# Kernel tuning notes

Hardware: AMD Instinct MI355X
Metric: run time of the kernel (lower is better)

## Reference

```python
import jax, jax.numpy as jnp
import numpy as np

B, N, C = 8, 729, 1152
H, D = 16, 72          # num_heads, head_dim (C = H*D)
F = 4304               # intermediate_size
R = 23                 # ToMe merge count r
EPS = 1e-6
SCALE = D ** -0.5


def _ln(x, g, b):
    m = jnp.mean(x, axis=-1, keepdims=True)
    v = jnp.var(x, axis=-1, keepdims=True)
    return (x - m) * jax.lax.rsqrt(v + EPS) * g + b


def _tome_merge_wavg(metric, x, r):
    """ToMe bipartite soft matching + weighted-average merge (size=None -> ones).
    metric: [B,N,D] per-token key mean; x: [B,N,C]. Returns [B, N-r, C]."""
    m = metric / jnp.linalg.norm(metric, axis=-1, keepdims=True)
    a, bm = m[:, ::2], m[:, 1::2]                       # [B,Na,D],[B,Nb,D]
    scores = jnp.einsum('bnd,bmd->bnm', a, bm)          # cosine sims [B,Na,Nb]
    node_max = jnp.max(scores, axis=-1)                 # [B,Na]
    node_idx = jnp.argmax(scores, axis=-1)              # best dst per src
    edge_idx = jnp.argsort(-node_max, axis=-1)          # descending similarity
    unm_idx = edge_idx[:, r:]                           # unmerged src tokens
    src_idx = edge_idx[:, :r]                           # merged src tokens
    dst_idx = jnp.take_along_axis(node_idx, src_idx, axis=1)  # [B,r]

    size = jnp.ones(x.shape[:2] + (1,), x.dtype)

    def merge_sum(t):
        src, dst = t[:, ::2], t[:, 1::2]
        unm = jnp.take_along_axis(src, unm_idx[..., None], axis=1)
        sel = jnp.take_along_axis(src, src_idx[..., None], axis=1)
        dst = jax.vmap(lambda d, i, s: d.at[i].add(s))(dst, dst_idx, sel)
        return jnp.concatenate([unm, dst], axis=1)

    xs = merge_sum(x * size)
    ss = merge_sum(size)
    return xs / ss


def setup_inputs() -> dict:
    key = jax.random.key(0)
    ks = jax.random.split(key, 16)
    s = 0.02
    inp = {
        'hidden_states': jax.random.normal(ks[0], (B, N, C), jnp.float32),
        'attention_mask': 0.1 * jax.random.normal(ks[1], (B, 1, N, N), jnp.float32),
        'wq': s * jax.random.normal(ks[2], (C, C), jnp.float32),
        'bq': jnp.zeros((C,), jnp.float32),
        'wk': s * jax.random.normal(ks[3], (C, C), jnp.float32),
        'bk': jnp.zeros((C,), jnp.float32),
        'wv': s * jax.random.normal(ks[4], (C, C), jnp.float32),
        'bv': jnp.zeros((C,), jnp.float32),
        'wo': s * jax.random.normal(ks[5], (C, C), jnp.float32),
        'bo': jnp.zeros((C,), jnp.float32),
        'ln1_w': jnp.ones((C,), jnp.float32),
        'ln1_b': jnp.zeros((C,), jnp.float32),
        'ln2_w': jnp.ones((C,), jnp.float32),
        'ln2_b': jnp.zeros((C,), jnp.float32),
        'fc1_w': s * jax.random.normal(ks[6], (C, F), jnp.float32),
        'fc1_b': jnp.zeros((F,), jnp.float32),
        'fc2_w': s * jax.random.normal(ks[7], (F, C), jnp.float32),
        'fc2_b': jnp.zeros((C,), jnp.float32),
    }
    return inp


def reference(hidden_states, attention_mask, wq, bq, wk, bk, wv, bv, wo, bo,
              ln1_w, ln1_b, ln2_w, ln2_b, fc1_w, fc1_b, fc2_w, fc2_b):
    residual = hidden_states
    x = _ln(hidden_states, ln1_w, ln1_b)

    q = (x @ wq + bq).reshape(B, N, H, D)
    k = (x @ wk + bk).reshape(B, N, H, D)
    v = (x @ wv + bv).reshape(B, N, H, D)

    metric = jnp.mean(k, axis=2)                        # [B,N,D] (mean over heads)

    scores = jnp.einsum('bqhd,bkhd->bhqk', q, k) * SCALE
    scores = scores + attention_mask                    # [B,1,N,N] broadcast bias
    attn = jax.nn.softmax(scores.astype(jnp.float32), axis=-1).astype(q.dtype)
    out = jnp.einsum('bhqk,bkhd->bqhd', attn, v).reshape(B, N, C)
    attn_out = out @ wo + bo

    h = residual + attn_out
    h = _tome_merge_wavg(metric, h, R)                  # [B, N-R, C]

    residual = h
    h = _ln(h, ln2_w, ln2_b)
    h = jax.nn.gelu(h @ fc1_w + fc1_b, approximate=True)  # gelu_pytorch_tanh
    h = h @ fc2_w + fc2_b
    return residual + h
```

## Files before the change

kernel.cpp:

```cpp
#include <hip/hip_runtime.h>
#include <hip/hip_bf16.h>
#include <math.h>

namespace {

constexpr int Bn = 8;
constexpr int Nn = 729;
constexpr int Cn = 1152;
constexpr int Hn = 16;
constexpr int Dn = 72;
constexpr int Fn = 4304;
constexpr int Rn = 23;
constexpr int NAn = 365;
constexpr int NBn = 364;
constexpr int NMn = 706;
constexpr int UNMn = NAn - Rn;
constexpr float EPSf = 1e-6f;
constexpr float SCALEf = 0.11785113019775793f;

using bf16 = __hip_bfloat16;
typedef short v8s __attribute__((ext_vector_type(8)));
typedef float v4f __attribute__((ext_vector_type(4)));

__device__ __forceinline__ float toF(bf16 v) { return __bfloat162float(v); }
__device__ __forceinline__ void stF(float* p, float v) { *p = v; }
__device__ __forceinline__ void stF(bf16* p, float v) { *p = __float2bfloat16(v); }

__device__ __forceinline__ float geluf(float x) {
  float x3 = x * x * x;
  return 0.5f * x * (1.f + tanhf(0.7978845608028654f * (x + 0.044715f * x3)));
}

__device__ __forceinline__ int clampi(int v, int lo, int hi) {
  return v < lo ? lo : (v > hi ? hi : v);
}

__global__ __launch_bounds__(256) void ln_stats_kernel(const float* __restrict__ x,
                                                       float* __restrict__ sf,
                                                       double* __restrict__ sd,
                                                       int rows) {
  int row = blockIdx.x;
  if (row >= rows) return;
  const float* xr = x + (size_t)row * Cn;
  double s = 0.0, s2 = 0.0;
  for (int c = threadIdx.x; c < Cn; c += 256) {
    double v = (double)xr[c];
    s += v; s2 += v * v;
  }
  __shared__ double sh[8];
#pragma unroll
  for (int o = 32; o > 0; o >>= 1) { s += __shfl_down(s, o); s2 += __shfl_down(s2, o); }
  int w = threadIdx.x >> 6;
  if ((threadIdx.x & 63) == 0) { sh[w] = s; sh[4 + w] = s2; }
  __syncthreads();
  if (threadIdx.x == 0) {
    double ts = sh[0] + sh[1] + sh[2] + sh[3];
    double ts2 = sh[4] + sh[5] + sh[6] + sh[7];
    double mean = ts / Cn;
    double var = ts2 / Cn - mean * mean;
    double rstd = 1.0 / sqrt(var + (double)EPSf);
    sf[2 * row] = (float)mean;
    sf[2 * row + 1] = (float)rstd;
    if (sd) { sd[2 * row] = mean; sd[2 * row + 1] = rstd; }
  }
}

__global__ __launch_bounds__(256) void ln_apply_kernel(const float* __restrict__ x,
                                                       const float* __restrict__ stats,
                                                       const float* __restrict__ g,
                                                       const float* __restrict__ b,
                                                       bf16* __restrict__ y) {
  int row = blockIdx.x;
  float mean = stats[2 * row], rstd = stats[2 * row + 1];
  const float* xr = x + (size_t)row * Cn;
  bf16* yr = y + (size_t)row * Cn;
  for (int c = threadIdx.x; c < Cn; c += 256)
    yr[c] = __float2bfloat16((xr[c] - mean) * rstd * g[c] + b[c]);
}

__global__ __launch_bounds__(256) void wconv_kernel(const float* __restrict__ W,
                                                    bf16* __restrict__ Wt,
                                                    int K, int N, float scale) {
  __shared__ float tile[32][33];
  int kt = blockIdx.y * 32, nt = blockIdx.x * 32;
  int tx = threadIdx.x & 31, ty = threadIdx.x >> 5;
#pragma unroll
  for (int yy = 0; yy < 4; ++yy) {
    int k = kt + ty * 4 + yy, n = nt + tx;
    tile[ty * 4 + yy][tx] = (k < K && n < N) ? W[(size_t)k * N + n] : 0.f;
  }
  __syncthreads();
#pragma unroll
  for (int yy = 0; yy < 4; ++yy) {
    int n = nt + ty * 4 + yy, k = kt + tx;
    if (n < N && k < K) Wt[(size_t)n * K + k] = __float2bfloat16(tile[tx][ty * 4 + yy] * scale);
  }
}

__global__ __launch_bounds__(256) void vscale_kernel(const float* __restrict__ in,
                                                     float* __restrict__ out, int n, float s) {
  int i = blockIdx.x * 256 + threadIdx.x;
  if (i < n) out[i] = in[i] * s;
}

template <typename OT, int BT>
__global__ __launch_bounds__(256) void mfma_gemm(const bf16* __restrict__ A,
                                                 const bf16* __restrict__ Wt,
                                                 const float* __restrict__ bias,
                                                 const float* __restrict__ resid,
                                                 OT* __restrict__ Cout,
                                                 int M, int N, int K, int act) {
  constexpr int FR = BT / 32;
  constexpr int PASSES = BT / 64;
  __align__(16) __shared__ short As[BT * 40];
  __align__(16) __shared__ short Bs[BT * 40];
  int bm = blockIdx.y * BT, bn = blockIdx.x * BT;
  int tid = threadIdx.x;
  int lane = tid & 63, w = tid >> 6;
  int wm = w >> 1, wn = w & 1;
  int l16 = lane & 15, quad = lane >> 4;
  int srow = tid >> 2, skc = (tid & 3) * 8;
  v4f acc[FR][FR];
#pragma unroll
  for (int i = 0; i < FR; ++i)
#pragma unroll
    for (int j = 0; j < FR; ++j) acc[i][j] = (v4f){0.f, 0.f, 0.f, 0.f};
  int ksteps = (K + 31) / 32;
  for (int ks = 0; ks < ksteps; ++ks) {
    int k0 = ks * 32;
    __syncthreads();
#pragma unroll
    for (int h = 0; h < PASSES; ++h) {
      int r = srow + h * 64;
      int4 za = {0, 0, 0, 0}, zb = {0, 0, 0, 0};
      if (k0 + skc < K) {
        if (bm + r < M) za = *reinterpret_cast<const int4*>(A + (size_t)(bm + r) * K + k0 + skc);
        if (bn + r < N) zb = *reinterpret_cast<const int4*>(Wt + (size_t)(bn + r) * K + k0 + skc);
      }
      *reinterpret_cast<int4*>(&As[r * 40 + skc]) = za;
      *reinterpret_cast<int4*>(&Bs[r * 40 + skc]) = zb;
    }
    __syncthreads();
    v8s af[FR], bfr[FR];
#pragma unroll
    for (int i = 0; i < FR; ++i)
      af[i] = *reinterpret_cast<const v8s*>(&As[(wm * (BT / 2) + i * 16 + l16) * 40 + quad * 8]);
#pragma unroll
    for (int j = 0; j < FR; ++j)
      bfr[j] = *reinterpret_cast<const v8s*>(&Bs[(wn * (BT / 2) + j * 16 + l16) * 40 + quad * 8]);
#pragma unroll
    for (int i = 0; i < FR; ++i)
#pragma unroll
      for (int j = 0; j < FR; ++j)
        acc[i][j] = __builtin_amdgcn_mfma_f32_16x16x32_bf16(af[i], bfr[j], acc[i][j], 0, 0, 0);
  }
#pragma unroll
  for (int i = 0; i < FR; ++i) {
#pragma unroll
    for (int j = 0; j < FR; ++j) {
#pragma unroll
      for (int r = 0; r < 4; ++r) {
        int row = bm + wm * (BT / 2) + i * 16 + quad * 4 + r;
        int col = bn + wn * (BT / 2) + j * 16 + l16;
        if (row < M && col < N) {
          float v = acc[i][j][r] + bias[col];
          if (act) v = geluf(v);
          if (resid) v += resid[(size_t)row * N + col];
          stF(&Cout[(size_t)row * N + col], v);
        }
      }
    }
  }
}

constexpr int NKP = 768;
__global__ __launch_bounds__(256) void vtrans_kernel(const bf16* __restrict__ v,
                                                     bf16* __restrict__ vt) {
  int kb = blockIdx.x % 12;
  int bh = blockIdx.x / 12;
  int h = bh % Hn, b = bh / Hn;
  __shared__ short Ts[64][73];
  int tid = threadIdx.x;
#pragma unroll
  for (int i = 0; i < 18; ++i) {
    int idx = tid + i * 256;
    int key = idx / 72, d = idx % 72;
    int kg = kb * 64 + key;
    bf16 val = (kg < Nn) ? v[((size_t)(b * Nn + kg)) * Cn + h * Dn + d] : bf16(0.f);
    Ts[key][d] = *reinterpret_cast<short*>(&val);
  }
  __syncthreads();
#pragma unroll
  for (int i = 0; i < 18; ++i) {
    int idx = tid + i * 256;
    int d = idx / 64, key = idx % 64;
    vt[((size_t)bh * 80 + d) * NKP + kb * 64 + key] = *reinterpret_cast<bf16*>(&Ts[key][d]);
  }
  for (int i = tid; i < 8 * 64; i += 256) {
    int d = 72 + i / 64, key = i % 64;
    vt[((size_t)bh * 80 + d) * NKP + kb * 64 + key] = bf16(0.f);
  }
}

constexpr int ATQ = 64, ATK = 64;
constexpr int NQT2 = (Nn + ATQ - 1) / ATQ;
constexpr int NKT = 12;
constexpr int KSS = 104, VTS = 72, PSS = 72;

__device__ __forceinline__ void attn_load_tile(const bf16* __restrict__ k,
                                               const bf16* __restrict__ vt,
                                               int b, int bh, int h, int kt_, int tid,
                                               int4* kr, int4* vr) {
#pragma unroll
  for (int i = 0; i < 3; ++i) {
    int idx = tid + i * 256;
    int r = idx / 12, ch = idx % 12;
    int kg = kt_ + r;
    int4 z = {0, 0, 0, 0};
    if (ch < 9 && kg < Nn)
      z = *reinterpret_cast<const int4*>(k + ((size_t)(b * Nn + kg)) * Cn + h * Dn + ch * 8);
    kr[i] = z;
    if (idx < 640) {
      int d = idx >> 3, kc = idx & 7;
      vr[i] = *reinterpret_cast<const int4*>(vt + ((size_t)bh * 80 + d) * NKP + kt_ + kc * 8);
    }
  }
}

__global__ __launch_bounds__(256) void attn_mfma_kernel(bf16* q ,
                                                        const bf16* __restrict__ k,
                                                        const bf16* __restrict__ vt,
                                                        const float* __restrict__ mask) {
  int blk = blockIdx.x;
  int qt = blk % NQT2;
  int bh = blk / NQT2;
  int h = bh % Hn;
  int b = bh / Hn;
  __align__(16) __shared__ short Ks[ATK * KSS];
  __align__(16) __shared__ short Vt[80 * VTS];
  __align__(16) __shared__ short Ps[4][16 * PSS];
  int tid = threadIdx.x;
  int lane = tid & 63, w = tid >> 6;
  int l16 = lane & 15, quad = lane >> 4;

  v8s aq[3];
  int qg_l = qt * ATQ + w * 16 + l16;
  {
    const bf16* qrow = q + ((size_t)(b * Nn + (qg_l < Nn ? qg_l : 0))) * Cn + h * Dn;
#pragma unroll
    for (int ks = 0; ks < 3; ++ks) {
      bool valid = (qg_l < Nn) && (ks < 2 || quad == 0);
      if (valid)
        aq[ks] = *reinterpret_cast<const v8s*>(qrow + ks * 32 + quad * 8);
      else
        aq[ks] = (v8s){0, 0, 0, 0, 0, 0, 0, 0};
    }
  }

  v4f o[5];
#pragma unroll
  for (int dj = 0; dj < 5; ++dj) o[dj] = (v4f){0.f, 0.f, 0.f, 0.f};
  float m_r[4] = {-INFINITY, -INFINITY, -INFINITY, -INFINITY};
  float l_r[4] = {0.f, 0.f, 0.f, 0.f};

  int4 kr[3], vr[3];
  attn_load_tile(k, vt, b, bh, h, 0, tid, kr, vr);

  for (int t = 0; t < NKT; ++t) {
    int kt2 = t * ATK;
    __syncthreads();
#pragma unroll
    for (int i = 0; i < 3; ++i) {
      int idx = tid + i * 256;
      int r = idx / 12, ch = idx % 12;
      *reinterpret_cast<int4*>(&Ks[r * KSS + ch * 8]) = kr[i];
      if (idx < 640) {
        int d = idx >> 3, kc = idx & 7;
        *reinterpret_cast<int4*>(&Vt[d * VTS + kc * 8]) = vr[i];
      }
    }
    __syncthreads();
    if (t + 1 < NKT) attn_load_tile(k, vt, b, bh, h, kt2 + ATK, tid, kr, vr);

    v4f sfr[4];
#pragma unroll
    for (int j = 0; j < 4; ++j) sfr[j] = (v4f){0.f, 0.f, 0.f, 0.f};
#pragma unroll
    for (int ks = 0; ks < 3; ++ks) {
#pragma unroll
      for (int j = 0; j < 4; ++j) {
        v8s bk_ = *reinterpret_cast<const v8s*>(&Ks[(j * 16 + l16) * KSS + ks * 32 + quad * 8]);
        sfr[j] = __builtin_amdgcn_mfma_f32_16x16x32_bf16(aq[ks], bk_, sfr[j], 0, 0, 0);
      }
    }
    float sv[4][4];
    int qbase = qt * ATQ + w * 16 + quad * 4;
    bool tfull = (kt2 + ATK <= Nn);
#pragma unroll
    for (int r = 0; r < 4; ++r) {
      int qg = qbase + r;
      const float* mrow = mask + ((size_t)(b * Nn + (qg < Nn ? qg : 0))) * Nn;
      if (tfull && qg < Nn) {
#pragma unroll
        for (int j = 0; j < 4; ++j) sv[j][r] = sfr[j][r] + mrow[kt2 + j * 16 + l16];
      } else {
#pragma unroll
        for (int j = 0; j < 4; ++j) {
          int kg = kt2 + j * 16 + l16;
          sv[j][r] = (kg < Nn && qg < Nn) ? sfr[j][r] + mrow[kg] : -INFINITY;
        }
      }
    }
    float alpha[4];
#pragma unroll
    for (int r = 0; r < 4; ++r) {
      float mx = fmaxf(fmaxf(sv[0][r], sv[1][r]), fmaxf(sv[2][r], sv[3][r]));
#pragma unroll
      for (int o2 = 1; o2 < 16; o2 <<= 1) mx = fmaxf(mx, __shfl_xor(mx, o2));
      float mnew = fmaxf(m_r[r], mx);
      float ps = 0.f;
#pragma unroll
      for (int j = 0; j < 4; ++j) {
        float p = __expf(sv[j][r] - mnew);
        bf16 pb = __float2bfloat16(p);
        Ps[w][(quad * 4 + r) * PSS + j * 16 + l16] = *reinterpret_cast<short*>(&pb);
        ps += p;
      }
#pragma unroll
      for (int o2 = 1; o2 < 16; o2 <<= 1) ps += __shfl_xor(ps, o2);
      alpha[r] = __expf(m_r[r] - mnew);
      l_r[r] = l_r[r] * alpha[r] + ps;
      m_r[r] = mnew;
    }
#pragma unroll
    for (int dj = 0; dj < 5; ++dj)
#pragma unroll
      for (int r = 0; r < 4; ++r) o[dj][r] *= alpha[r];
#pragma unroll
    for (int st = 0; st < 2; ++st) {
      v8s ap = *reinterpret_cast<const v8s*>(&Ps[w][l16 * PSS + st * 32 + quad * 8]);
#pragma unroll
      for (int dj = 0; dj < 5; ++dj) {
        v8s bv_ = *reinterpret_cast<const v8s*>(&Vt[(dj * 16 + l16) * VTS + st * 32 + quad * 8]);
        o[dj] = __builtin_amdgcn_mfma_f32_16x16x32_bf16(ap, bv_, o[dj], 0, 0, 0);
      }
    }
  }
  float linv[4];
#pragma unroll
  for (int r = 0; r < 4; ++r) linv[r] = (l_r[r] > 0.f) ? 1.f / l_r[r] : 0.f;
#pragma unroll
  for (int dj = 0; dj < 5; ++dj) {
    int d = dj * 16 + l16;
    if (d >= Dn) continue;
#pragma unroll
    for (int r = 0; r < 4; ++r) {
      int qg = qt * ATQ + w * 16 + quad * 4 + r;
      if (qg < Nn)
        q[((size_t)(b * Nn + qg)) * Cn + h * Dn + d] = __float2bfloat16(o[dj][r] * linv[r]);
    }
  }
}

__global__ __launch_bounds__(128) void wkavg_kernel(const float* __restrict__ wk,
                                                    const float* __restrict__ bk,
                                                    double* __restrict__ wka,
                                                    double* __restrict__ bka) {
  int c = blockIdx.x;
  int d = threadIdx.x;
  if (d < Dn) {
    double s = 0.0;
    for (int h = 0; h < Hn; ++h) s += (double)wk[(size_t)c * Cn + h * Dn + d];
    wka[(size_t)c * Dn + d] = s / Hn;
    if (c == 0) {
      double t = 0.0;
      for (int h = 0; h < Hn; ++h) t += (double)bk[h * Dn + d];
      bka[d] = t / Hn;
    }
  }
}

constexpr int MT_ROWS = 64;
constexpr int MT_KT = 32;
constexpr int MT_SK = 3;
constexpr int MT_KC = Cn / MT_SK;
__global__ __launch_bounds__(256) void metric_gemm_kernel(const float* __restrict__ x,
                                                          const double* __restrict__ sd,
                                                          const float* __restrict__ g,
                                                          const float* __restrict__ b,
                                                          const double* __restrict__ wka,
                                                          double* __restrict__ kpart,
                                                          int rows) {
  int row0 = blockIdx.x * MT_ROWS;
  int k0base = blockIdx.y * MT_KC;
  __shared__ double As[MT_ROWS][MT_KT + 1];
  __shared__ double Ws[MT_KT][Dn];
  __shared__ double smean[MT_ROWS], srstd[MT_ROWS];
  int tid = threadIdx.x;
  int rg = tid >> 3;
  int dg = tid & 7;
  int d0 = dg * 9;
  if (tid < MT_ROWS) {
    int r = row0 + tid;
    smean[tid] = (r < rows) ? sd[2 * r] : 0.0;
    srstd[tid] = (r < rows) ? sd[2 * r + 1] : 0.0;
  }
  double acc0[9], acc1[9];
#pragma unroll
  for (int j = 0; j < 9; ++j) { acc0[j] = 0.0; acc1[j] = 0.0; }
  __syncthreads();
  for (int kt = 0; kt < MT_KC; kt += MT_KT) {
    int k0 = k0base + kt;
    __syncthreads();
#pragma unroll
    for (int i = 0; i < 8; ++i) {
      int idx = tid + i * 256;
      int c = idx & 31, r = idx >> 5;
      int gr = row0 + r;
      double a = 0.0;
      if (gr < rows) {
        double xv = (double)x[(size_t)gr * Cn + k0 + c];
        a = (xv - smean[r]) * srstd[r] * (double)g[k0 + c] + (double)b[k0 + c];
      }
      As[r][c] = a;
    }
#pragma unroll
    for (int i = 0; i < 9; ++i) {
      int idx = tid + i * 256;
      int c = idx / Dn, d = idx % Dn;
      Ws[c][d] = wka[(size_t)(k0 + c) * Dn + d];
    }
    __syncthreads();
#pragma unroll 2
    for (int c = 0; c < MT_KT; ++c) {
      double a0 = As[rg * 2][c], a1 = As[rg * 2 + 1][c];
#pragma unroll
      for (int j = 0; j < 9; ++j) {
        double wv = Ws[c][d0 + j];
        acc0[j] += a0 * wv;
        acc1[j] += a1 * wv;
      }
    }
  }
  size_t base = (size_t)blockIdx.y * rows;
  int r0g = row0 + rg * 2;
#pragma unroll
  for (int j = 0; j < 9; ++j) {
    if (r0g < rows) kpart[(base + r0g) * Dn + d0 + j] = acc0[j];
    if (r0g + 1 < rows) kpart[(base + r0g + 1) * Dn + d0 + j] = acc1[j];
  }
}

__global__ __launch_bounds__(128) void metric_norm_kernel(const double* __restrict__ kpart,
                                                          const double* __restrict__ bka,
                                                          double* __restrict__ mn,
                                                          int rows) {
  int row = blockIdx.x;
  __shared__ double red[Dn];
  __shared__ double nrm;
  int d = threadIdx.x;
  double v = 0.0;
  if (d < Dn) {
    v = kpart[(size_t)row * Dn + d]
      + kpart[((size_t)rows + row) * Dn + d]
      + kpart[((size_t)2 * rows + row) * Dn + d]
      + bka[d];
    red[d] = v * v;
  }
  __syncthreads();
  if (threadIdx.x == 0) {
    double t = 0.0;
    for (int i = 0; i < Dn; ++i) t += red[i];
    nrm = 1.0 / sqrt(t > 0.0 ? t : 1e-300);
  }
  __syncthreads();
  if (d < Dn) mn[(size_t)row * Dn + d] = v * nrm;
}

__global__ __launch_bounds__(128) void tome_score_kernel(const double* __restrict__ mn,
                                                         double* __restrict__ nmax,
                                                         int* __restrict__ nidx) {
  int blk = blockIdx.x;
  int i = blk % NAn;
  int b = blk / NAn;
  __shared__ double av[Dn];
  __shared__ double sv[128];
  __shared__ int si[128];
  int tid = threadIdx.x;
  if (tid < Dn) av[tid] = mn[((size_t)(b * Nn) + 2 * i) * Dn + tid];
  __syncthreads();
  double best = -1e300;
  int bi = 0;
  for (int c2 = tid; c2 < NBn; c2 += 128) {
    const double* bv = mn + ((size_t)(b * Nn) + 2 * c2 + 1) * Dn;
    double s = 0.0;
#pragma unroll 8
    for (int dd = 0; dd < Dn; ++dd) s += av[dd] * bv[dd];
    if (s > best) { best = s; bi = c2; }
  }
  sv[tid] = best;
  si[tid] = bi;
  __syncthreads();
  if (tid == 0) {
    double bb = sv[0];
    int ii = si[0];
    for (int t2 = 1; t2 < 128; ++t2) {
      if (sv[t2] > bb || (sv[t2] == bb && si[t2] < ii)) { bb = sv[t2]; ii = si[t2]; }
    }
    nmax[b * NAn + i] = bb;
    nidx[b * NAn + i] = clampi(ii, 0, NBn - 1);
  }
}

__global__ __launch_bounds__(512) void tome_sort_kernel(const double* __restrict__ nmax,
                                                        const int* __restrict__ nidx,
                                                        int* __restrict__ unm,
                                                        int* __restrict__ srcI,
                                                        int* __restrict__ dstI,
                                                        float* __restrict__ cnt) {
  int b = blockIdx.x;
  __shared__ double v[NAn];
  __shared__ int eidx[NAn];
  __shared__ int dsts[Rn];
  int tid = threadIdx.x;
  for (int i = tid; i < NAn; i += blockDim.x) {
    v[i] = nmax[b * NAn + i];
    eidx[i] = i;
  }
  __syncthreads();
  for (int i = tid; i < NAn; i += blockDim.x) {
    double vi = v[i];
    int rank = 0;
    for (int j = 0; j < NAn; ++j) {
      double vj = v[j];
      rank += (vj > vi) || (vj == vi && j < i);
    }
    eidx[clampi(rank, 0, NAn - 1)] = i;
  }
  __syncthreads();
  for (int r2 = tid; r2 < NAn; r2 += blockDim.x) {
    if (r2 >= Rn) unm[(size_t)b * UNMn + (r2 - Rn)] = clampi(eidx[r2], 0, NAn - 1);
  }
  if (tid < Rn) {
    int s = clampi(eidx[tid], 0, NAn - 1);
    srcI[b * Rn + tid] = s;
    int dd = clampi(nidx[b * NAn + s], 0, NBn - 1);
    dsts[tid] = dd;
    dstI[b * Rn + tid] = dd;
  }
  for (int j = tid; j < NBn; j += blockDim.x) cnt[(size_t)b * NBn + j] = 1.f;
  __syncthreads();
  if (tid == 0) {
    for (int r2 = 0; r2 < Rn; ++r2) cnt[(size_t)b * NBn + dsts[r2]] += 1.f;
  }
}

__global__ __launch_bounds__(256) void tome_merge_kernel(const float* __restrict__ h,
                                                         const int* __restrict__ unm,
                                                         const int* __restrict__ srcI,
                                                         const int* __restrict__ dstI,
                                                         const float* __restrict__ cnt,
                                                         float* __restrict__ mg) {
  int blk = blockIdx.x;
  int t = blk % NMn;
  int b = blk / NMn;
  __shared__ int s_src[Rn], s_dst[Rn];
  if (threadIdx.x < Rn) {
    s_src[threadIdx.x] = clampi(srcI[b * Rn + threadIdx.x], 0, NAn - 1);
    s_dst[threadIdx.x] = clampi(dstI[b * Rn + threadIdx.x], 0, NBn - 1);
  }
  __syncthreads();
  if (t < UNMn) {
    int tok = clampi(2 * clampi(unm[(size_t)b * UNMn + t], 0, NAn - 1), 0, Nn - 1);
    for (int c = threadIdx.x; c < Cn; c += 256)
      mg[((size_t)(b * NMn + t)) * Cn + c] = h[((size_t)(b * Nn + tok)) * Cn + c];
  } else {
    int j = t - UNMn;
    int tok = 2 * j + 1;
    float inv = 1.f / cnt[b * NBn + j];
    for (int c = threadIdx.x; c < Cn; c += 256) {
      float vsum = h[((size_t)(b * Nn + tok)) * Cn + c];
      for (int r2 = 0; r2 < Rn; ++r2)
        if (s_dst[r2] == j) vsum += h[((size_t)(b * Nn + 2 * s_src[r2])) * Cn + c];
      mg[((size_t)(b * NMn + t)) * Cn + c] = vsum * inv;
    }
  }
}

inline int cdiv(int a, int b) { return (a + b - 1) / b; }

}

extern "C" void kernel_launch(void* const* d_in, const int* in_sizes, int n_in,
                              void* d_out, int out_size, void* d_ws, size_t ws_size,
                              hipStream_t stream) {
  const float* hidden = (const float*)d_in[0];
  const float* mask   = (const float*)d_in[1];
  const float* wq = (const float*)d_in[2];
  const float* bq = (const float*)d_in[3];
  const float* wk = (const float*)d_in[4];
  const float* bk = (const float*)d_in[5];
  const float* wv = (const float*)d_in[6];
  const float* bv = (const float*)d_in[7];
  const float* wo = (const float*)d_in[8];
  const float* bo = (const float*)d_in[9];
  const float* ln1w = (const float*)d_in[10];
  const float* ln1b = (const float*)d_in[11];
  const float* ln2w = (const float*)d_in[12];
  const float* ln2b = (const float*)d_in[13];
  const float* fc1w = (const float*)d_in[14];
  const float* fc1b = (const float*)d_in[15];
  const float* fc2w = (const float*)d_in[16];
  const float* fc2b = (const float*)d_in[17];
  float* out = (float*)d_out;
  (void)in_sizes; (void)n_in; (void)out_size; (void)ws_size;

  char* ws = (char*)d_ws;
  size_t off = 0;
  auto alloc = [&](size_t nbytes) -> void* {
    void* p = ws + off;
    off += (nbytes + 255) & ~(size_t)255;
    return p;
  };
  int rows = Bn * Nn;
  int mrows = Bn * NMn;
  size_t bnc = (size_t)rows * Cn;
  bf16* wqT = (bf16*)alloc((size_t)Cn * Cn * 2);
  bf16* wkT = (bf16*)alloc((size_t)Cn * Cn * 2);
  bf16* wvT = (bf16*)alloc((size_t)Cn * Cn * 2);
  bf16* woT = (bf16*)alloc((size_t)Cn * Cn * 2);
  bf16* fc1T = (bf16*)alloc((size_t)Fn * Cn * 2);
  bf16* fc2T = (bf16*)alloc((size_t)Cn * Fn * 2);
  bf16* xlnB = (bf16*)alloc(bnc * 2);
  bf16* qb = (bf16*)alloc(bnc * 2);
  bf16* kb = (bf16*)alloc(bnc * 2);
  bf16* vb = (bf16*)alloc(bnc * 2);
  bf16* h2B = (bf16*)alloc((size_t)mrows * Cn * 2);
  constexpr int CHUNK = 2824;
  bf16* ffnB = (bf16*)alloc((size_t)CHUNK * Fn * 2);
  double* mnD = (double*)alloc((size_t)rows * Dn * 8);
  double* wkavgD = (double*)alloc((size_t)Cn * Dn * 8);
  double* bkavgD = (double*)alloc((size_t)Dn * 8);
  float* stats1f = (float*)alloc((size_t)rows * 2 * 4);
  double* stats1d = (double*)alloc((size_t)rows * 2 * 8);
  float* stats2f = (float*)alloc((size_t)mrows * 2 * 4);
  double* nmaxD = (double*)alloc((size_t)Bn * NAn * 8);
  int* nidx = (int*)alloc((size_t)Bn * NAn * 4);
  int* unm  = (int*)alloc((size_t)Bn * UNMn * 4);
  int* srcI = (int*)alloc((size_t)Bn * Rn * 4);
  int* dstI = (int*)alloc((size_t)Bn * Rn * 4);
  float* cnt = (float*)alloc((size_t)Bn * NBn * 4);
  float* bqS = (float*)alloc((size_t)Cn * 4);
  float* hbuf = (float*)kb;
  float* mg   = (float*)xlnB;
  bf16* vtG   = ffnB;
  double* kpartD = (double*)ffnB;

  wconv_kernel<<<dim3(cdiv(Cn, 32), cdiv(Cn, 32)), 256, 0, stream>>>(wq, wqT, Cn, Cn, SCALEf);
  wconv_kernel<<<dim3(cdiv(Cn, 32), cdiv(Cn, 32)), 256, 0, stream>>>(wk, wkT, Cn, Cn, 1.f);
  wconv_kernel<<<dim3(cdiv(Cn, 32), cdiv(Cn, 32)), 256, 0, stream>>>(wv, wvT, Cn, Cn, 1.f);
  wconv_kernel<<<dim3(cdiv(Cn, 32), cdiv(Cn, 32)), 256, 0, stream>>>(wo, woT, Cn, Cn, 1.f);
  wconv_kernel<<<dim3(cdiv(Fn, 32), cdiv(Cn, 32)), 256, 0, stream>>>(fc1w, fc1T, Cn, Fn, 1.f);
  wconv_kernel<<<dim3(cdiv(Cn, 32), cdiv(Fn, 32)), 256, 0, stream>>>(fc2w, fc2T, Fn, Cn, 1.f);
  vscale_kernel<<<cdiv(Cn, 256), 256, 0, stream>>>(bq, bqS, Cn, SCALEf);

  ln_stats_kernel<<<rows, 256, 0, stream>>>(hidden, stats1f, stats1d, rows);

  wkavg_kernel<<<Cn, 128, 0, stream>>>(wk, bk, wkavgD, bkavgD);
  metric_gemm_kernel<<<dim3(cdiv(rows, MT_ROWS), MT_SK), 256, 0, stream>>>(
      hidden, stats1d, ln1w, ln1b, wkavgD, kpartD, rows);
  metric_norm_kernel<<<rows, 128, 0, stream>>>(kpartD, bkavgD, mnD, rows);
  tome_score_kernel<<<Bn * NAn, 128, 0, stream>>>(mnD, nmaxD, nidx);
  tome_sort_kernel<<<Bn, 512, 0, stream>>>(nmaxD, nidx, unm, srcI, dstI, cnt);

  ln_apply_kernel<<<rows, 256, 0, stream>>>(hidden, stats1f, ln1w, ln1b, xlnB);

  dim3 g64(cdiv(Cn, 64), cdiv(rows, 64));
  mfma_gemm<bf16, 64><<<g64, 256, 0, stream>>>(xlnB, wqT, bqS, nullptr, qb, rows, Cn, Cn, 0);
  mfma_gemm<bf16, 64><<<g64, 256, 0, stream>>>(xlnB, wkT, bk, nullptr, kb, rows, Cn, Cn, 0);
  mfma_gemm<bf16, 64><<<g64, 256, 0, stream>>>(xlnB, wvT, bv, nullptr, vb, rows, Cn, Cn, 0);

  vtrans_kernel<<<Bn * Hn * 12, 256, 0, stream>>>(vb, vtG);

  attn_mfma_kernel<<<Bn * Hn * NQT2, 256, 0, stream>>>(qb, kb, vtG, mask);

  mfma_gemm<float, 64><<<g64, 256, 0, stream>>>(qb, woT, bo, hidden, hbuf, rows, Cn, Cn, 0);

  tome_merge_kernel<<<Bn * NMn, 256, 0, stream>>>(hbuf, unm, srcI, dstI, cnt, mg);

  ln_stats_kernel<<<mrows, 256, 0, stream>>>(mg, stats2f, (double*)nullptr, mrows);
  ln_apply_kernel<<<mrows, 256, 0, stream>>>(mg, stats2f, ln2w, ln2b, h2B);

  for (int c0 = 0; c0 < mrows; c0 += CHUNK) {
    int m = (mrows - c0 < CHUNK) ? (mrows - c0) : CHUNK;
    dim3 gf1(cdiv(Fn, 128), cdiv(m, 128));
    mfma_gemm<bf16, 128><<<gf1, 256, 0, stream>>>(h2B + (size_t)c0 * Cn, fc1T, fc1b, nullptr,
                                                  ffnB, m, Fn, Cn, 1);
    dim3 gf2(cdiv(Cn, 64), cdiv(m, 64));
    mfma_gemm<float, 64><<<gf2, 256, 0, stream>>>(ffnB, fc2T, fc2b, mg + (size_t)c0 * Cn,
                                                  out + (size_t)c0 * Cn, m, Cn, Fn, 0);
  }
}
```

Measured before the change: 1.174 ms.

## Use direct global-to-LDS loads in GEMM, remap attention blocks, enlarge FFN chunk

The GEMM tile loader now issues global_load_lds 16-byte transfers straight into unpadded shared memory for interior tiles, skipping the register round trip. Edge tiles keep the old guarded path. Removing the 40-short row padding may add LDS bank conflicts on fragment reads. The attention kernel interleaves batch as the fastest block index, which should change L2 locality for the mask. The per-iteration row-sum shuffle reduction is deferred to the end, and the FFN chunk size grows to all rows when the workspace is large enough, cutting chunk launches.

```diff
diff --git a/kernel.cpp b/kernel.cpp
--- a/kernel.cpp
+++ b/kernel.cpp
@@ -35,6 +35,12 @@
   return v < lo ? lo : (v > hi ? hi : v);
 }
 
+__device__ __forceinline__ void gl_lds16(const bf16* __restrict__ g, short* l) {
+  __builtin_amdgcn_global_load_lds(
+      (const __attribute__((address_space(1))) void*)g,
+      (__attribute__((address_space(3))) void*)l, 16, 0, 0);
+}
+
 __global__ __launch_bounds__(256) void ln_stats_kernel(const float* __restrict__ x,
                                                        float* __restrict__ sf,
                                                        double* __restrict__ sd,
@@ -111,15 +117,17 @@
                                                  OT* __restrict__ Cout,
                                                  int M, int N, int K, int act) {
   constexpr int FR = BT / 32;
-  constexpr int PASSES = BT / 64;
-  __align__(16) __shared__ short As[BT * 40];
-  __align__(16) __shared__ short Bs[BT * 40];
+  constexpr int WL = BT / 64;
+  __align__(16) __shared__ short As[BT * 32];
+  __align__(16) __shared__ short Bs[BT * 32];
   int bm = blockIdx.y * BT, bn = blockIdx.x * BT;
   int tid = threadIdx.x;
   int lane = tid & 63, w = tid >> 6;
   int wm = w >> 1, wn = w & 1;
   int l16 = lane & 15, quad = lane >> 4;
   int srow = tid >> 2, skc = (tid & 3) * 8;
+  int lr = lane >> 2, lc8 = (lane & 3) * 8;
+  bool interior = (bm + BT <= M) && (bn + BT <= N);
   v4f acc[FR][FR];
 #pragma unroll
   for (int i = 0; i < FR; ++i)
@@ -129,25 +137,35 @@
   for (int ks = 0; ks < ksteps; ++ks) {
     int k0 = ks * 32;
     __syncthreads();
-#pragma unroll
-    for (int h = 0; h < PASSES; ++h) {
-      int r = srow + h * 64;
-      int4 za = {0, 0, 0, 0}, zb = {0, 0, 0, 0};
-      if (k0 + skc < K) {
-        if (bm + r < M) za = *reinterpret_cast<const int4*>(A + (size_t)(bm + r) * K + k0 + skc);
-        if (bn + r < N) zb = *reinterpret_cast<const int4*>(Wt + (size_t)(bn + r) * K + k0 + skc);
-      }
-      *reinterpret_cast<int4*>(&As[r * 40 + skc]) = za;
-      *reinterpret_cast<int4*>(&Bs[r * 40 + skc]) = zb;
+    if (interior && (k0 + 32 <= K)) {
+#pragma unroll
+      for (int h2 = 0; h2 < WL; ++h2) {
+        int rb = (w + h2 * 4) * 16;
+        int r = rb + lr;
+        gl_lds16(A + (size_t)(bm + r) * K + k0 + lc8, &As[rb * 32]);
+        gl_lds16(Wt + (size_t)(bn + r) * K + k0 + lc8, &Bs[rb * 32]);
+      }
+    } else {
+#pragma unroll
+      for (int h2 = 0; h2 < WL; ++h2) {
+        int r = srow + h2 * 64;
+        int4 za = {0, 0, 0, 0}, zb = {0, 0, 0, 0};
+        if (k0 + skc < K) {
+          if (bm + r < M) za = *reinterpret_cast<const int4*>(A + (size_t)(bm + r) * K + k0 + skc);
+          if (bn + r < N) zb = *reinterpret_cast<const int4*>(Wt + (size_t)(bn + r) * K + k0 + skc);
+        }
+        *reinterpret_cast<int4*>(&As[r * 32 + skc]) = za;
+        *reinterpret_cast<int4*>(&Bs[r * 32 + skc]) = zb;
+      }
     }
     __syncthreads();
     v8s af[FR], bfr[FR];
 #pragma unroll
     for (int i = 0; i < FR; ++i)
-      af[i] = *reinterpret_cast<const v8s*>(&As[(wm * (BT / 2) + i * 16 + l16) * 40 + quad * 8]);
+      af[i] = *reinterpret_cast<const v8s*>(&As[(wm * (BT / 2) + i * 16 + l16) * 32 + quad * 8]);
 #pragma unroll
     for (int j = 0; j < FR; ++j)
-      bfr[j] = *reinterpret_cast<const v8s*>(&Bs[(wn * (BT / 2) + j * 16 + l16) * 40 + quad * 8]);
+      bfr[j] = *reinterpret_cast<const v8s*>(&Bs[(wn * (BT / 2) + j * 16 + l16) * 32 + quad * 8]);
 #pragma unroll
     for (int i = 0; i < FR; ++i)
 #pragma unroll
@@ -232,10 +250,11 @@
                                                         const bf16* __restrict__ vt,
                                                         const float* __restrict__ mask) {
   int blk = blockIdx.x;
-  int qt = blk % NQT2;
-  int bh = blk / NQT2;
-  int h = bh % Hn;
-  int b = bh / Hn;
+  int b = blk & 7;
+  int r0 = blk >> 3;
+  int h = r0 / NQT2;
+  int qt = r0 % NQT2;
+  int bh = b * Hn + h;
   __align__(16) __shared__ short Ks[ATK * KSS];
   __align__(16) __shared__ short Vt[80 * VTS];
   __align__(16) __shared__ short Ps[4][16 * PSS];
@@ -326,8 +345,6 @@
         Ps[w][(quad * 4 + r) * PSS + j * 16 + l16] = *reinterpret_cast<short*>(&pb);
         ps += p;
       }
-#pragma unroll
-      for (int o2 = 1; o2 < 16; o2 <<= 1) ps += __shfl_xor(ps, o2);
       alpha[r] = __expf(m_r[r] - mnew);
       l_r[r] = l_r[r] * alpha[r] + ps;
       m_r[r] = mnew;
@@ -348,7 +365,12 @@
   }
   float linv[4];
 #pragma unroll
-  for (int r = 0; r < 4; ++r) linv[r] = (l_r[r] > 0.f) ? 1.f / l_r[r] : 0.f;
+  for (int r = 0; r < 4; ++r) {
+    float lt = l_r[r];
+#pragma unroll
+    for (int o2 = 1; o2 < 16; o2 <<= 1) lt += __shfl_xor(lt, o2);
+    linv[r] = (lt > 0.f) ? 1.f / lt : 0.f;
+  }
 #pragma unroll
   for (int dj = 0; dj < 5; ++dj) {
     int d = dj * 16 + l16;
@@ -613,7 +635,7 @@
   const float* fc2w = (const float*)d_in[16];
   const float* fc2b = (const float*)d_in[17];
   float* out = (float*)d_out;
-  (void)in_sizes; (void)n_in; (void)out_size; (void)ws_size;
+  (void)in_sizes; (void)n_in; (void)out_size;
 
   char* ws = (char*)d_ws;
   size_t off = 0;
@@ -636,8 +658,6 @@
   bf16* kb = (bf16*)alloc(bnc * 2);
   bf16* vb = (bf16*)alloc(bnc * 2);
   bf16* h2B = (bf16*)alloc((size_t)mrows * Cn * 2);
-  constexpr int CHUNK = 2824;
-  bf16* ffnB = (bf16*)alloc((size_t)CHUNK * Fn * 2);
   double* mnD = (double*)alloc((size_t)rows * Dn * 8);
   double* wkavgD = (double*)alloc((size_t)Cn * Dn * 8);
   double* bkavgD = (double*)alloc((size_t)Dn * 8);
@@ -651,6 +671,10 @@
   int* dstI = (int*)alloc((size_t)Bn * Rn * 4);
   float* cnt = (float*)alloc((size_t)Bn * NBn * 4);
   float* bqS = (float*)alloc((size_t)Cn * 4);
+  bf16* ffnB = (bf16*)(ws + off);
+  size_t remain = (ws_size > off) ? (ws_size - off) : 0;
+  size_t fullB = (size_t)mrows * Fn * 2;
+  int CHUNK = (remain >= fullB) ? mrows : 2824;
   float* hbuf = (float*)kb;
   float* mg   = (float*)xlnB;
   bf16* vtG   = ffnB;
```

New measurement: 1.133 ms. 3.5% less time.
